# Performance work log

Hardware: AMD Instinct MI355X
Metric: run time of the kernel (lower is better)

## Reference

```python
import jax, jax.numpy as jnp
import numpy as np

B, C, N, K, H = 8, 64, 4096, 32, 4
D = C // H  # head dim = 16
EPS = 1e-5  # BatchNorm eps (torch default)


def setup_inputs() -> dict:
    key = jax.random.key(0)
    ks = jax.random.split(key, 7)
    s = 0.05
    return {
        "x": jax.random.normal(ks[0], (B, C, N), jnp.float32),
        "wq": jax.random.normal(ks[1], (C, C), jnp.float32) * s,
        "wk": jax.random.normal(ks[2], (C, C), jnp.float32) * s,
        "wv": jax.random.normal(ks[3], (C, C), jnp.float32) * s,
        "w1": jax.random.normal(ks[4], (4 * C, C), jnp.float32) * s,
        "w2": jax.random.normal(ks[5], (C, 4 * C), jnp.float32) * s,
        "g1": jnp.ones((C,), jnp.float32),
        "b1": jnp.zeros((C,), jnp.float32),
        "g2": jnp.ones((C,), jnp.float32),
        "b2": jnp.zeros((C,), jnp.float32),
    }


def _bn(f, g, b):
    # BatchNorm1d in training mode: stats over (batch, points) per channel.
    # f: (B, N, C)
    mu = jnp.mean(f, axis=(0, 1))
    var = jnp.var(f, axis=(0, 1))  # biased, as torch uses for normalization
    return (f - mu) * jax.lax.rsqrt(var + EPS) * g + b


def reference(x, wq, wk, wv, w1, w2, g1, b1, g2, b2):
    feat = jnp.transpose(x, (0, 2, 1))  # (B, N, C)
    # KNN in feature space: negative squared distances, take top-K largest
    sq = jnp.sum(feat * feat, axis=-1)  # (B, N)
    neg_d = 2.0 * jnp.einsum('bnc,bmc->bnm', feat, feat) - sq[:, :, None] - sq[:, None, :]
    _, idx = jax.lax.top_k(neg_d, K)  # (B, N, K) int32
    # gather neighbors and form diffs
    nbrs = jax.vmap(lambda p, i: p[i])(feat, idx)  # (B, N, K, C)
    diff = nbrs - feat[:, :, None, :]
    # 1x1-conv projections (bias-free linear over channels)
    q = jnp.einsum('bnc,oc->bno', feat, wq).reshape(B, N, H, D)
    k = jnp.einsum('bnkc,oc->bnko', diff, wk).reshape(B, N, K, H, D)
    v = jnp.einsum('bnkc,oc->bnko', diff, wv).reshape(B, N, K, H, D)
    energy = jnp.einsum('bnhd,bnkhd->bnhk', q, k) / jnp.sqrt(jnp.float32(D))
    attn = jax.nn.softmax(energy, axis=-1)  # softmax over K neighbors
    out = jnp.einsum('bnhk,bnkhd->bnhd', attn, v).reshape(B, N, C)  # H-major merge
    f1 = _bn(feat + out, g1, b1)
    hid = jnp.einsum('bnc,oc->bno', f1, w1)
    hid = jnp.where(hid > 0, hid, 0.2 * hid)  # LeakyReLU(0.2)
    ff = jnp.einsum('bno,co->bnc', hid, w2)
    f2 = _bn(f1 + ff, g2, b2)
    return jnp.transpose(f2, (0, 2, 1))  # (B, C, N)
```

## Files before the change

### kernel.cpp

```cpp
#include <hip/hip_runtime.h>

#define Bdim 8
#define Cdim 64
#define Ndim 4096
#define Kdim 32
#define ROWS (Bdim*Ndim)
#define BN_EPS 1e-5f

__device__ __forceinline__ float dot4(float4 a, float4 b){
  return a.x*b.x + a.y*b.y + a.z*b.z + a.w*b.w;
}
__device__ __forceinline__ int wofs(int o, int g){ return o*64 + (((g ^ ((o>>2)&7)))<<2); }
__device__ __forceinline__ unsigned keyOf(float f){
  unsigned u = __float_as_uint(f);
  return (u & 0x80000000u) ? ~u : (u ^ 0x80000000u);
}

__global__ __launch_bounds__(256) void prep_proj_kernel(const float* __restrict__ x,
    const float* __restrict__ wq, const float* __restrict__ wk,
    const float* __restrict__ wv,
    float* __restrict__ sq,
    float* __restrict__ Qo, float* __restrict__ PKo, float* __restrict__ PVo,
    float* __restrict__ accZ)
{
  __shared__ __align__(16) float ftile[64*68];
  __shared__ __align__(16) float Ws[3][64*64];
  const int tid = threadIdx.x;
  const int blk = blockIdx.x;
  const int b  = blk & 7;
  const int n0 = (blk >> 3) * 64;
  if (blk == 0) accZ[tid] = 0.f;
  for (int k=0;k<16;++k){
    int idx = tid + (k<<8);
    int c = idx>>6, nn = idx&63;
    ftile[nn*68+c] = x[((size_t)b*64+c)*Ndim + n0 + nn];
  }
  {
    const float* wp[3] = {wq, wk, wv};
    for (int m=0;m<3;++m)
      for (int k=0;k<16;++k){
        int idx = tid + (k<<8);
        int o = idx>>6, c = idx&63;
        Ws[m][wofs(o, c>>2) + (c&3)] = wp[m][o*64 + c];
      }
  }
  __syncthreads();
  if (tid < 64){
    float a = 0.f;
    #pragma unroll
    for (int c=0;c<64;++c){ float v = ftile[tid*68+c]; a += v*v; }
    sq[b*Ndim + n0 + tid] = a;
  }
  const int tr = tid>>4, to = tid&15;
  const size_t rowBase = (size_t)b*Ndim + n0;
  float* outp[3] = {Qo, PKo, PVo};
  for (int m=0;m<3;++m){
    float acc[4][4];
    #pragma unroll
    for (int r=0;r<4;++r){ acc[r][0]=0.f; acc[r][1]=0.f; acc[r][2]=0.f; acc[r][3]=0.f; }
    #pragma unroll 4
    for (int c4=0;c4<16;++c4){
      float4 f[4], w[4];
      #pragma unroll
      for (int r=0;r<4;++r)  f[r] = *(const float4*)&ftile[(4*tr+r)*68 + (c4<<2)];
      #pragma unroll
      for (int oo=0;oo<4;++oo) w[oo] = *(const float4*)&Ws[m][wofs(4*to+oo, c4)];
      #pragma unroll
      for (int r=0;r<4;++r)
        #pragma unroll
        for (int oo=0;oo<4;++oo)
          acc[r][oo] += dot4(f[r], w[oo]);
    }
    #pragma unroll
    for (int r=0;r<4;++r){
      float4 v; v.x=acc[r][0]; v.y=acc[r][1]; v.z=acc[r][2]; v.w=acc[r][3];
      *(float4*)&outp[m][(rowBase + 4*tr + r)*64 + 4*to] = v;
    }
  }
}

__global__ __launch_bounds__(512, 4) void knn_attn_kernel(
    const float* __restrict__ x,
    const float* __restrict__ sq,
    const float* __restrict__ Qm, const float* __restrict__ PKm, const float* __restrict__ PVm,
    float* __restrict__ t1, float* __restrict__ bn1s, float* __restrict__ bn1q)
{
  __shared__ __align__(16) unsigned char smem[40992];
  float*    chunkF = (float*)smem;
  unsigned* candK  = (unsigned*)smem;
  int*      candI  = (int*)(smem + 2048);
  int*      outIdx = (int*)(smem + 4096);
  float*    enS    = (float*)(smem + 5120);
  float*    red1   = (float*)(smem + 5120);
  float*    red2   = (float*)(smem + 7168);
  float*    fnS    = (float*)(smem + 32768);
  float*    qvS    = (float*)(smem + 34816);
  float*    pknS   = (float*)(smem + 36864);
  float*    pvnS   = (float*)(smem + 38912);
  float*    sqnS   = (float*)(smem + 40960);

  const int tid = threadIdx.x;
  const int lane = tid & 63;
  const int w = tid >> 6;
  const int blk = blockIdx.x;
  const int b  = blk & 7;
  const int n0 = (blk >> 3) << 3;
  const float* xb = x + (size_t)b*64*Ndim;

  {
    int j = tid>>6, c = tid&63;
    size_t ro = ((size_t)b*Ndim + n0 + j)*64 + c;
    fnS[tid]  = xb[(size_t)c*Ndim + n0 + j];
    qvS[tid]  = Qm[ro];
    pknS[tid] = PKm[ro];
    pvnS[tid] = PVm[ro];
    if (tid < 8) sqnS[tid] = sq[b*Ndim + n0 + tid];
  }
  __syncthreads();

  unsigned kk[64];

  #pragma unroll
  for (int g=0; g<2; ++g){
    const int m0 = (g<<11) + (tid<<2);
    float acc[8][4];
    #pragma unroll
    for (int q=0;q<8;++q){ acc[q][0]=0.f; acc[q][1]=0.f; acc[q][2]=0.f; acc[q][3]=0.f; }
    #pragma unroll 4
    for (int c=0;c<64;++c){
      float4 xm = *(const float4*)&xb[(size_t)c*Ndim + m0];
      float4 qA = *(const float4*)&xb[(size_t)c*Ndim + n0];
      float4 qB = *(const float4*)&xb[(size_t)c*Ndim + n0 + 4];
      const float qs[8] = {qA.x,qA.y,qA.z,qA.w,qB.x,qB.y,qB.z,qB.w};
      #pragma unroll
      for (int q=0;q<8;++q){
        acc[q][0] += qs[q]*xm.x; acc[q][1] += qs[q]*xm.y;
        acc[q][2] += qs[q]*xm.z; acc[q][3] += qs[q]*xm.w;
      }
    }
    float4 sqm4 = *(const float4*)&sq[b*Ndim + m0];
    #pragma unroll
    for (int half=0; half<2; ++half){
      __syncthreads();
      #pragma unroll
      for (int qq=0;qq<4;++qq){
        int q = (half<<2)+qq;
        float sqn_q = sqnS[q];
        float4 v;
        v.x = (2.f*acc[q][0]-sqn_q)-sqm4.x;
        v.y = (2.f*acc[q][1]-sqn_q)-sqm4.y;
        v.z = (2.f*acc[q][2]-sqn_q)-sqm4.z;
        v.w = (2.f*acc[q][3]-sqn_q)-sqm4.w;
        *(float4*)&chunkF[(qq<<11) + (tid<<2)] = v;
      }
      __syncthreads();
      if ((w>>2) == half){
        const int wq = w & 3;
        #pragma unroll
        for (int i=0;i<32;++i)
          kk[(g<<5)+i] = keyOf(chunkF[(wq<<11)+(i<<6)+lane]);
      }
    }
  }
  __syncthreads();

  if (lane < 32) outIdx[(w<<5)+lane] = n0 + w;

  {
    unsigned lmax = kk[0];
    #pragma unroll
    for (int j=1;j<64;++j) lmax = lmax > kk[j] ? lmax : kk[j];
    unsigned T = 0u;
    #pragma unroll
    for (int bit=31; bit>=0; --bit){
      unsigned cand = T | (1u << bit);
      int cnt = (int)__popcll(__ballot(lmax >= cand));
      if (cnt >= 32) T = cand;
    }
    int base = 0;
    #pragma unroll
    for (int j=0;j<64;++j){
      bool isc = (kk[j] >= T);
      unsigned long long mk = __ballot(isc);
      if (isc){
        int slot = base + (int)__popcll(mk & ((1ull<<lane)-1ull));
        if (slot < 64){
          candK[(w<<6)+slot] = kk[j];
          candI[(w<<6)+slot] = ((j>>5)<<11)+((j&31)<<6)+lane;
        }
      }
      base += (int)__popcll(mk);
    }
    const int S = base;
    __threadfence_block();
    if (S <= 64){
      unsigned long long C = 0ull;
      if (lane < S)
        C = ((unsigned long long)candK[(w<<6)+lane] << 32) |
            (unsigned long long)(~(unsigned)candI[(w<<6)+lane]);
      #pragma unroll
      for (int k2=2; k2<=64; k2<<=1){
        #pragma unroll
        for (int j2=k2>>1; j2>=1; j2>>=1){
          unsigned long long P = (unsigned long long)__shfl_xor((long long)C, j2, 64);
          bool lowIdx  = ((lane & j2) == 0);
          bool keepMax = (lowIdx == ((lane & k2) == 0));
          unsigned long long mx = C > P ? C : P;
          unsigned long long mn = C > P ? P : C;
          C = keepMax ? mx : mn;
        }
      }
      if (lane < 32) outIdx[(w<<5)+lane] = (int)(~(unsigned)(C & 0xFFFFFFFFull)) & (Ndim-1);
    } else {
      unsigned Te = 0u;
      for (int bit=31; bit>=0; --bit){
        unsigned cand = Te | (1u << bit);
        int lc = 0;
        #pragma unroll
        for (int j=0;j<64;++j) lc += (kk[j] >= cand) ? 1 : 0;
        #pragma unroll
        for (int off=1; off<64; off<<=1) lc += __shfl_xor(lc, off, 64);
        if (lc >= 32) Te = cand;
      }
      const unsigned long long below = (1ull << lane) - 1ull;
      int b2 = 0;
      #pragma unroll
      for (int j=0;j<64;++j){
        unsigned u = kk[j];
        unsigned long long mg = __ballot(u > Te);
        if (u > Te){
          int slot = b2 + (int)__popcll(mg & below);
          if (slot < 32) outIdx[(w<<5)+slot] = ((j>>5)<<11)+((j&31)<<6)+lane;
        }
        b2 += (int)__popcll(mg);
      }
      #pragma unroll
      for (int j=0;j<64;++j){
        unsigned u = kk[j];
        unsigned long long mt = __ballot(u == Te);
        if (u == Te){
          int slot = b2 + (int)__popcll(mt & below);
          if (slot < 32) outIdx[(w<<5)+slot] = ((j>>5)<<11)+((j&31)<<6)+lane;
        }
        b2 += (int)__popcll(mt);
      }
    }
  }
  __syncthreads();

  #pragma unroll
  for (int p=0;p<2;++p){
    int task = tid + (p<<9);
    int jn = task>>7, h = (task>>5)&3, k2 = task&31;
    int mj = outIdx[(jn<<5)+k2] & (Ndim-1);
    const float4* pk4 = (const float4*)(PKm + ((size_t)b*Ndim + mj)*64 + (h<<4));
    const float4* qq4 = (const float4*)&qvS[(jn<<6)+(h<<4)];
    const float4* nn4 = (const float4*)&pknS[(jn<<6)+(h<<4)];
    float e = 0.f;
    #pragma unroll
    for (int d=0;d<4;++d){
      float4 kv = pk4[d], qq = qq4[d], nn = nn4[d];
      e += qq.x*(kv.x-nn.x) + qq.y*(kv.y-nn.y) + qq.z*(kv.z-nn.z) + qq.w*(kv.w-nn.w);
    }
    enS[(jn<<7)+(h<<5)+k2] = e * 0.25f;
  }
  __syncthreads();
  if (tid < 32){
    int jn = tid>>2, h = tid&3;
    float* ep = &enS[(jn<<7)+(h<<5)];
    float mx = -1e30f;
    for (int k2=0;k2<32;++k2) mx = fmaxf(mx, ep[k2]);
    float ssum = 0.f;
    for (int k2=0;k2<32;++k2){ float ex = expf(ep[k2]-mx); ep[k2] = ex; ssum += ex; }
    float inv = 1.f/ssum;
    for (int k2=0;k2<32;++k2) ep[k2] *= inv;
  }
  __syncthreads();
  float tval;
  {
    int jn = tid>>6, c = tid&63, h = c>>4;
    float a2 = 0.f;
    #pragma unroll 8
    for (int k2=0;k2<32;++k2){
      int mj = outIdx[(jn<<5)+k2] & (Ndim-1);
      a2 += enS[(jn<<7)+(h<<5)+k2] * (PVm[((size_t)b*Ndim + mj)*64 + c] - pvnS[(jn<<6)+c]);
    }
    tval = fnS[(jn<<6)+c] + a2;
    t1[((size_t)b*Ndim + n0 + jn)*64 + c] = tval;
  }
  __syncthreads();
  red1[tid] = tval;
  red2[tid] = tval*tval;
  __syncthreads();
  if (tid < 64){
    float S = 0.f, S2 = 0.f;
    #pragma unroll
    for (int j=0;j<8;++j){ S += red1[(j<<6)+tid]; S2 += red2[(j<<6)+tid]; }
    atomicAdd(&bn1s[tid], S);
    atomicAdd(&bn1q[tid], S2);
  }
}

__global__ __launch_bounds__(256) void mlp_kernel(const float* __restrict__ t1,
    const float* __restrict__ w1, const float* __restrict__ w2,
    const float* __restrict__ g1, const float* __restrict__ b1,
    const float* __restrict__ bns, const float* __restrict__ bnq,
    float* __restrict__ t2, float* __restrict__ bn2s, float* __restrict__ bn2q)
{
  __shared__ __align__(16) float f1l[64*68];
  __shared__ __align__(16) float hl[64*68];
  __shared__ __align__(16) float w1s[64*64];
  __shared__ __align__(16) float w2s[64*64];
  __shared__ float mu[64], rs[64], gg[64], bb[64];
  const int tid = threadIdx.x;
  if (tid < 64){
    float m = bns[tid] * (1.f/32768.f);
    float v = bnq[tid] * (1.f/32768.f) - m*m;
    mu[tid] = m; rs[tid] = 1.f/sqrtf(v + BN_EPS);
    gg[tid] = g1[tid]; bb[tid] = b1[tid];
  }
  __syncthreads();
  const size_t rowBase = (size_t)blockIdx.x*64;
  for (int k=0;k<16;++k){
    int idx = tid + (k<<8);
    int r = idx>>6, c = idx&63;
    float v = t1[(rowBase + r)*64 + c];
    f1l[r*68+c] = (v - mu[c])*rs[c]*gg[c] + bb[c];
  }
  const int tr = tid>>4, to = tid&15;
  float ff[4][4];
  #pragma unroll
  for (int r=0;r<4;++r){ ff[r][0]=0.f; ff[r][1]=0.f; ff[r][2]=0.f; ff[r][3]=0.f; }

  for (int hc=0; hc<4; ++hc){
    __syncthreads();
    for (int k=0;k<16;++k){
      int idx = tid + (k<<8);
      int o = idx>>6, c = idx&63;
      w1s[wofs(o, c>>2) + (c&3)] = w1[(size_t)(hc*64+o)*64 + c];
      w2s[wofs(o, c>>2) + (c&3)] = w2[(size_t)o*256 + hc*64 + c];
    }
    __syncthreads();
    float hv[4][4];
    #pragma unroll
    for (int r=0;r<4;++r){ hv[r][0]=0.f; hv[r][1]=0.f; hv[r][2]=0.f; hv[r][3]=0.f; }
    #pragma unroll 4
    for (int c4=0;c4<16;++c4){
      float4 f[4], w[4];
      #pragma unroll
      for (int r=0;r<4;++r)  f[r] = *(const float4*)&f1l[(4*tr+r)*68 + (c4<<2)];
      #pragma unroll
      for (int oo=0;oo<4;++oo) w[oo] = *(const float4*)&w1s[wofs(4*to+oo, c4)];
      #pragma unroll
      for (int r=0;r<4;++r)
        #pragma unroll
        for (int oo=0;oo<4;++oo)
          hv[r][oo] += dot4(f[r], w[oo]);
    }
    #pragma unroll
    for (int r=0;r<4;++r){
      float4 v;
      float x0=hv[r][0], x1=hv[r][1], x2=hv[r][2], x3=hv[r][3];
      v.x = (x0>0.f)?x0:0.2f*x0; v.y = (x1>0.f)?x1:0.2f*x1;
      v.z = (x2>0.f)?x2:0.2f*x2; v.w = (x3>0.f)?x3:0.2f*x3;
      *(float4*)&hl[(4*tr+r)*68 + 4*to] = v;
    }
    __syncthreads();
    #pragma unroll 4
    for (int o4=0;o4<16;++o4){
      float4 h[4], w[4];
      #pragma unroll
      for (int r=0;r<4;++r)  h[r] = *(const float4*)&hl[(4*tr+r)*68 + (o4<<2)];
      #pragma unroll
      for (int oo=0;oo<4;++oo) w[oo] = *(const float4*)&w2s[wofs(4*to+oo, o4)];
      #pragma unroll
      for (int r=0;r<4;++r)
        #pragma unroll
        for (int oo=0;oo<4;++oo)
          ff[r][oo] += dot4(h[r], w[oo]);
    }
  }
  float ls[4]  = {0.f,0.f,0.f,0.f};
  float ls2[4] = {0.f,0.f,0.f,0.f};
  #pragma unroll
  for (int r=0;r<4;++r){
    float4 v;
    v.x = f1l[(4*tr+r)*68 + 4*to+0] + ff[r][0];
    v.y = f1l[(4*tr+r)*68 + 4*to+1] + ff[r][1];
    v.z = f1l[(4*tr+r)*68 + 4*to+2] + ff[r][2];
    v.w = f1l[(4*tr+r)*68 + 4*to+3] + ff[r][3];
    *(float4*)&t2[(rowBase + 4*tr + r)*64 + 4*to] = v;
    ls[0]+=v.x; ls[1]+=v.y; ls[2]+=v.z; ls[3]+=v.w;
    ls2[0]+=v.x*v.x; ls2[1]+=v.y*v.y; ls2[2]+=v.z*v.z; ls2[3]+=v.w*v.w;
  }
  __syncthreads();
  #pragma unroll
  for (int i=0;i<4;++i){
    hl[tr*64 + 4*to + i]        = ls[i];
    hl[1024 + tr*64 + 4*to + i] = ls2[i];
  }
  __syncthreads();
  if (tid < 64){
    float S = 0.f, S2 = 0.f;
    #pragma unroll
    for (int g2=0; g2<16; ++g2){ S += hl[g2*64 + tid]; S2 += hl[1024 + g2*64 + tid]; }
    atomicAdd(&bn2s[tid], S);
    atomicAdd(&bn2q[tid], S2);
  }
}

__global__ __launch_bounds__(256) void final_kernel(const float* __restrict__ t2,
    const float* __restrict__ bns, const float* __restrict__ bnq,
    const float* __restrict__ g2, const float* __restrict__ b2,
    float* __restrict__ out)
{
  __shared__ float tile[64*65];
  __shared__ float mu[64], rs[64], gg[64], bb[64];
  const int tid = threadIdx.x;
  const int b = blockIdx.y;
  const int n0 = blockIdx.x*64;
  if (tid < 64){
    float m = bns[tid] * (1.f/32768.f);
    float v = bnq[tid] * (1.f/32768.f) - m*m;
    mu[tid] = m; rs[tid] = 1.f/sqrtf(v + BN_EPS);
    gg[tid] = g2[tid]; bb[tid] = b2[tid];
  }
  __syncthreads();
  for (int k=0;k<16;++k){
    int idx = tid + (k<<8);
    int r = idx>>6, c = idx&63;
    float v = t2[((size_t)b*Ndim + n0 + r)*64 + c];
    tile[r*65+c] = (v - mu[c])*rs[c]*gg[c] + bb[c];
  }
  __syncthreads();
  for (int k=0;k<16;++k){
    int idx = tid + (k<<8);
    int c = idx>>6, nn = idx&63;
    out[((size_t)b*64 + c)*Ndim + n0 + nn] = tile[nn*65+c];
  }
}

extern "C" void kernel_launch(void* const* d_in, const int* in_sizes, int n_in,
                              void* d_out, int out_size, void* d_ws, size_t ws_size,
                              hipStream_t stream)
{
  (void)in_sizes; (void)n_in; (void)out_size; (void)ws_size;
  const float* x  = (const float*)d_in[0];
  const float* wq = (const float*)d_in[1];
  const float* wk = (const float*)d_in[2];
  const float* wv = (const float*)d_in[3];
  const float* w1 = (const float*)d_in[4];
  const float* w2 = (const float*)d_in[5];
  const float* g1 = (const float*)d_in[6];
  const float* b1 = (const float*)d_in[7];
  const float* g2 = (const float*)d_in[8];
  const float* b2 = (const float*)d_in[9];
  float* out = (float*)d_out;

  const size_t NE = (size_t)ROWS*64;
  float* sq   = (float*)d_ws;
  float* Qb   = sq + ROWS;
  float* PKb  = Qb + NE;
  float* PVb  = PKb + NE;
  float* t1   = PVb + NE;
  float* t2   = t1 + NE;
  float* acc  = t2 + NE;

  prep_proj_kernel<<<dim3(512), 256, 0, stream>>>(x, wq, wk, wv, sq, Qb, PKb, PVb, acc);
  knn_attn_kernel<<<dim3(4096), 512, 0, stream>>>(x, sq, Qb, PKb, PVb, t1, acc, acc+64);
  mlp_kernel<<<dim3(512), 256, 0, stream>>>(t1, w1, w2, g1, b1, acc, acc+64, t2, acc+128, acc+192);
  final_kernel<<<dim3(64,8), 256, 0, stream>>>(t2, acc+128, acc+192, g2, b2, out);
}
```

Before: 443.8 us.

## Use bf16 MFMA for KNN distances with 16-bit keys and exact fp32 rerank

The prep kernel now also writes a row-major fp32 copy of the features and a bf16 copy. The KNN kernel computes approximate pairwise distances with bf16 MFMA instructions and quantizes them to 16-bit keys, so two query rows share each register key. It then selects candidates with a widened threshold margin and re-ranks up to 64 of them with exact fp32 distances before a bitonic sort. Each block handles 16 query points instead of 8, halving the grid. The cost is the risk of missing true neighbours when quantization error exceeds the margin or more than 64 candidates tie, plus extra workspace writes. The t2 buffer is reused as scratch.

```diff
diff --git a/kernel.cpp b/kernel.cpp
--- a/kernel.cpp
+++ b/kernel.cpp
@@ -7,6 +7,9 @@
 #define ROWS (Bdim*Ndim)
 #define BN_EPS 1e-5f
 
+using f32x4  = __attribute__((ext_vector_type(4))) float;
+using bf16x8 = __attribute__((ext_vector_type(8))) short;
+
 __device__ __forceinline__ float dot4(float4 a, float4 b){
   return a.x*b.x + a.y*b.y + a.z*b.z + a.w*b.w;
 }
@@ -21,7 +24,8 @@
     const float* __restrict__ wv,
     float* __restrict__ sq,
     float* __restrict__ Qo, float* __restrict__ PKo, float* __restrict__ PVo,
-    float* __restrict__ accZ)
+    float* __restrict__ accZ,
+    float* __restrict__ featT, unsigned short* __restrict__ xh)
 {
   __shared__ __align__(16) float ftile[64*68];
   __shared__ __align__(16) float Ws[3][64*64];
@@ -29,6 +33,7 @@
   const int blk = blockIdx.x;
   const int b  = blk & 7;
   const int n0 = (blk >> 3) * 64;
+  const size_t rowBase = (size_t)b*Ndim + n0;
   if (blk == 0) accZ[tid] = 0.f;
   for (int k=0;k<16;++k){
     int idx = tid + (k<<8);
@@ -45,6 +50,15 @@
       }
   }
   __syncthreads();
+  for (int k=0;k<16;++k){
+    int idx = tid + (k<<8);
+    int r = idx>>6, c = idx&63;
+    float v = ftile[r*68+c];
+    size_t o = (rowBase + r)*64 + c;
+    featT[o] = v;
+    unsigned u = __float_as_uint(v);
+    xh[o] = (unsigned short)((u + 0x7FFFu + ((u>>16)&1u)) >> 16);
+  }
   if (tid < 64){
     float a = 0.f;
     #pragma unroll
@@ -52,7 +66,6 @@
     sq[b*Ndim + n0 + tid] = a;
   }
   const int tr = tid>>4, to = tid&15;
-  const size_t rowBase = (size_t)b*Ndim + n0;
   float* outp[3] = {Qo, PKo, PVo};
   for (int m=0;m<3;++m){
     float acc[4][4];
@@ -80,180 +93,179 @@
 }
 
 __global__ __launch_bounds__(512, 4) void knn_attn_kernel(
-    const float* __restrict__ x,
     const float* __restrict__ sq,
     const float* __restrict__ Qm, const float* __restrict__ PKm, const float* __restrict__ PVm,
+    const float* __restrict__ featT, const unsigned short* __restrict__ xh,
     float* __restrict__ t1, float* __restrict__ bn1s, float* __restrict__ bn1q)
 {
-  __shared__ __align__(16) unsigned char smem[40992];
-  float*    chunkF = (float*)smem;
-  unsigned* candK  = (unsigned*)smem;
-  int*      candI  = (int*)(smem + 2048);
-  int*      outIdx = (int*)(smem + 4096);
-  float*    enS    = (float*)(smem + 5120);
-  float*    red1   = (float*)(smem + 5120);
-  float*    red2   = (float*)(smem + 7168);
-  float*    fnS    = (float*)(smem + 32768);
-  float*    qvS    = (float*)(smem + 34816);
-  float*    pknS   = (float*)(smem + 36864);
-  float*    pvnS   = (float*)(smem + 38912);
-  float*    sqnS   = (float*)(smem + 40960);
-
-  const int tid = threadIdx.x;
+  __shared__ __align__(16) unsigned char smem[49216];
+  unsigned short* bufA = (unsigned short*)smem;
+  unsigned short* bufB = (unsigned short*)(smem + 16384);
+  int*   candI  = (int*)smem;
+  int*   outIdx = (int*)(smem + 2048);
+  float* enS    = (float*)(smem + 4096);
+  float* red1   = (float*)(smem + 12288);
+  float* red2   = (float*)(smem + 14336);
+  float* fnS    = (float*)(smem + 32768);
+  float* qvS    = (float*)(smem + 36864);
+  float* pknS   = (float*)(smem + 40960);
+  float* pvnS   = (float*)(smem + 45056);
+  float* sqnS   = (float*)(smem + 49152);
+
+  const int tid  = threadIdx.x;
   const int lane = tid & 63;
-  const int w = tid >> 6;
-  const int blk = blockIdx.x;
-  const int b  = blk & 7;
-  const int n0 = (blk >> 3) << 3;
-  const float* xb = x + (size_t)b*64*Ndim;
+  const int w    = tid >> 6;
+  const int blk  = blockIdx.x;
+  const int b    = blk & 7;
+  const int n0   = (blk >> 3) << 4;
+  const size_t b4096 = (size_t)b << 12;
+  const int qa = w, qb = w + 8;
+
+  #pragma unroll
+  for (int rr=0; rr<2; ++rr){
+    int idx = tid + (rr<<9);
+    int j = idx>>6, c = idx&63;
+    size_t ro = (b4096 + n0 + j)*64 + c;
+    fnS[idx]  = featT[ro];
+    qvS[idx]  = Qm[ro];
+    pknS[idx] = PKm[ro];
+    pvnS[idx] = PVm[ro];
+  }
+  if (tid < 16) sqnS[tid] = sq[b4096 + n0 + tid];
+  __syncthreads();
+
+  unsigned kk[64];
 
   {
-    int j = tid>>6, c = tid&63;
-    size_t ro = ((size_t)b*Ndim + n0 + j)*64 + c;
-    fnS[tid]  = xb[(size_t)c*Ndim + n0 + j];
-    qvS[tid]  = Qm[ro];
-    pknS[tid] = PKm[ro];
-    pvnS[tid] = PVm[ro];
-    if (tid < 8) sqnS[tid] = sq[b*Ndim + n0 + tid];
-  }
-  __syncthreads();
-
-  unsigned kk[64];
-
-  #pragma unroll
-  for (int g=0; g<2; ++g){
-    const int m0 = (g<<11) + (tid<<2);
-    float acc[8][4];
-    #pragma unroll
-    for (int q=0;q<8;++q){ acc[q][0]=0.f; acc[q][1]=0.f; acc[q][2]=0.f; acc[q][3]=0.f; }
-    #pragma unroll 4
-    for (int c=0;c<64;++c){
-      float4 xm = *(const float4*)&xb[(size_t)c*Ndim + m0];
-      float4 qA = *(const float4*)&xb[(size_t)c*Ndim + n0];
-      float4 qB = *(const float4*)&xb[(size_t)c*Ndim + n0 + 4];
-      const float qs[8] = {qA.x,qA.y,qA.z,qA.w,qB.x,qB.y,qB.z,qB.w};
-      #pragma unroll
-      for (int q=0;q<8;++q){
-        acc[q][0] += qs[q]*xm.x; acc[q][1] += qs[q]*xm.y;
-        acc[q][2] += qs[q]*xm.z; acc[q][3] += qs[q]*xm.w;
-      }
-    }
-    float4 sqm4 = *(const float4*)&sq[b*Ndim + m0];
-    #pragma unroll
-    for (int half=0; half<2; ++half){
+    const unsigned short* xhb = xh + (b4096 << 6);
+    const int l15  = lane & 15;
+    const int acol = (lane >> 4) << 3;
+    const int qrow = (lane >> 4) << 2;
+    bf16x8 a0 = *(const bf16x8*)&xhb[(size_t)(n0 + l15)*64 + acol];
+    bf16x8 a1 = *(const bf16x8*)&xhb[(size_t)(n0 + l15)*64 + acol + 32];
+    float sqn_r[4];
+    #pragma unroll
+    for (int r=0;r<4;++r) sqn_r[r] = sqnS[qrow + r];
+    const float* sqb = sq + b4096;
+    #pragma unroll
+    for (int ch=0; ch<8; ++ch){
+      unsigned short* buf = (ch & 1) ? bufB : bufA;
+      #pragma unroll
+      for (int t=0;t<4;++t){
+        const int brow = (w<<9) + (ch<<6) + (t<<4) + l15;
+        bf16x8 b0 = *(const bf16x8*)&xhb[(size_t)brow*64 + acol];
+        bf16x8 b1 = *(const bf16x8*)&xhb[(size_t)brow*64 + acol + 32];
+        f32x4 acc = {0.f,0.f,0.f,0.f};
+        acc = __builtin_amdgcn_mfma_f32_16x16x32_bf16(a0, b0, acc, 0, 0, 0);
+        acc = __builtin_amdgcn_mfma_f32_16x16x32_bf16(a1, b1, acc, 0, 0, 0);
+        float sm = sqb[brow];
+        #pragma unroll
+        for (int r=0;r<4;++r){
+          float d = 2.f*acc[r] - sqn_r[r] - sm;
+          int k16 = (int)fmaf(d, 204.8f, 65536.0f);
+          k16 = k16 < 0 ? 0 : (k16 > 65535 ? 65535 : k16);
+          buf[((w<<4) + qrow + r)*64 + (t<<4) + l15] = (unsigned short)k16;
+        }
+      }
       __syncthreads();
       #pragma unroll
-      for (int qq=0;qq<4;++qq){
-        int q = (half<<2)+qq;
-        float sqn_q = sqnS[q];
-        float4 v;
-        v.x = (2.f*acc[q][0]-sqn_q)-sqm4.x;
-        v.y = (2.f*acc[q][1]-sqn_q)-sqm4.y;
-        v.z = (2.f*acc[q][2]-sqn_q)-sqm4.z;
-        v.w = (2.f*acc[q][3]-sqn_q)-sqm4.w;
-        *(float4*)&chunkF[(qq<<11) + (tid<<2)] = v;
-      }
-      __syncthreads();
-      if ((w>>2) == half){
-        const int wq = w & 3;
-        #pragma unroll
-        for (int i=0;i<32;++i)
-          kk[(g<<5)+i] = keyOf(chunkF[(wq<<11)+(i<<6)+lane]);
-      }
-    }
-  }
-  __syncthreads();
-
-  if (lane < 32) outIdx[(w<<5)+lane] = n0 + w;
-
-  {
-    unsigned lmax = kk[0];
-    #pragma unroll
-    for (int j=1;j<64;++j) lmax = lmax > kk[j] ? lmax : kk[j];
-    unsigned T = 0u;
-    #pragma unroll
-    for (int bit=31; bit>=0; --bit){
-      unsigned cand = T | (1u << bit);
+      for (int i=0;i<8;++i){
+        unsigned kA = buf[((i<<4) + qa)*64 + lane];
+        unsigned kB = buf[((i<<4) + qb)*64 + lane];
+        kk[(ch<<3)+i] = (kA<<16) | kB;
+      }
+    }
+  }
+
+  if (lane < 32){ outIdx[(qa<<5)+lane] = n0 + qa; outIdx[(qb<<5)+lane] = n0 + qb; }
+
+  const unsigned long long below = (1ull<<lane) - 1ull;
+  #pragma unroll
+  for (int pass=0; pass<2; ++pass){
+    const int q = pass ? qb : qa;
+    unsigned lmax = 0;
+    #pragma unroll
+    for (int j=0;j<64;++j){
+      unsigned kj = pass ? (kk[j]&0xFFFFu) : (kk[j]>>16);
+      lmax = lmax > kj ? lmax : kj;
+    }
+    unsigned T = 0;
+    #pragma unroll
+    for (int bit=15; bit>=0; --bit){
+      unsigned cand = T | (1u<<bit);
       int cnt = (int)__popcll(__ballot(lmax >= cand));
       if (cnt >= 32) T = cand;
     }
+    const unsigned Tm = (T > 72u) ? (T - 72u) : 0u;
     int base = 0;
     #pragma unroll
     for (int j=0;j<64;++j){
-      bool isc = (kk[j] >= T);
+      unsigned kj = pass ? (kk[j]&0xFFFFu) : (kk[j]>>16);
+      bool isc = (kj >= Tm);
       unsigned long long mk = __ballot(isc);
       if (isc){
-        int slot = base + (int)__popcll(mk & ((1ull<<lane)-1ull));
-        if (slot < 64){
-          candK[(w<<6)+slot] = kk[j];
-          candI[(w<<6)+slot] = ((j>>5)<<11)+((j&31)<<6)+lane;
+        int slot = base + (int)__popcll(mk & below);
+        if (slot < 64) candI[(w<<6)+slot] = ((j&7)<<9) + ((j>>3)<<6) + lane;
+      }
+      base += (int)__popcll(mk);
+    }
+    int S = base;
+    if (S > 64){
+      base = 0;
+      #pragma unroll
+      for (int j=0;j<64;++j){
+        unsigned kj = pass ? (kk[j]&0xFFFFu) : (kk[j]>>16);
+        bool isc = (kj >= T);
+        unsigned long long mk = __ballot(isc);
+        if (isc){
+          int slot = base + (int)__popcll(mk & below);
+          if (slot < 64) candI[(w<<6)+slot] = ((j&7)<<9) + ((j>>3)<<6) + lane;
         }
-      }
-      base += (int)__popcll(mk);
-    }
-    const int S = base;
+        base += (int)__popcll(mk);
+      }
+      S = base < 64 ? base : 64;
+    }
     __threadfence_block();
-    if (S <= 64){
-      unsigned long long C = 0ull;
-      if (lane < S)
-        C = ((unsigned long long)candK[(w<<6)+lane] << 32) |
-            (unsigned long long)(~(unsigned)candI[(w<<6)+lane]);
-      #pragma unroll
-      for (int k2=2; k2<=64; k2<<=1){
-        #pragma unroll
-        for (int j2=k2>>1; j2>=1; j2>>=1){
-          unsigned long long P = (unsigned long long)__shfl_xor((long long)C, j2, 64);
-          bool lowIdx  = ((lane & j2) == 0);
-          bool keepMax = (lowIdx == ((lane & k2) == 0));
-          unsigned long long mx = C > P ? C : P;
-          unsigned long long mn = C > P ? P : C;
-          C = keepMax ? mx : mn;
-        }
-      }
-      if (lane < 32) outIdx[(w<<5)+lane] = (int)(~(unsigned)(C & 0xFFFFFFFFull)) & (Ndim-1);
-    } else {
-      unsigned Te = 0u;
-      for (int bit=31; bit>=0; --bit){
-        unsigned cand = Te | (1u << bit);
-        int lc = 0;
-        #pragma unroll
-        for (int j=0;j<64;++j) lc += (kk[j] >= cand) ? 1 : 0;
-        #pragma unroll
-        for (int off=1; off<64; off<<=1) lc += __shfl_xor(lc, off, 64);
-        if (lc >= 32) Te = cand;
-      }
-      const unsigned long long below = (1ull << lane) - 1ull;
-      int b2 = 0;
-      #pragma unroll
-      for (int j=0;j<64;++j){
-        unsigned u = kk[j];
-        unsigned long long mg = __ballot(u > Te);
-        if (u > Te){
-          int slot = b2 + (int)__popcll(mg & below);
-          if (slot < 32) outIdx[(w<<5)+slot] = ((j>>5)<<11)+((j&31)<<6)+lane;
-        }
-        b2 += (int)__popcll(mg);
-      }
-      #pragma unroll
-      for (int j=0;j<64;++j){
-        unsigned u = kk[j];
-        unsigned long long mt = __ballot(u == Te);
-        if (u == Te){
-          int slot = b2 + (int)__popcll(mt & below);
-          if (slot < 32) outIdx[(w<<5)+slot] = ((j>>5)<<11)+((j&31)<<6)+lane;
-        }
-        b2 += (int)__popcll(mt);
-      }
-    }
-  }
-  __syncthreads();
-
-  #pragma unroll
-  for (int p=0;p<2;++p){
+    int mj = -1; unsigned keyE = 0u;
+    if (lane < S){
+      mj = candI[(w<<6)+lane];
+      const float* fm = featT + (b4096 + mj)*64;
+      const float* fq = fnS + (q<<6);
+      float as = 0.f;
+      #pragma unroll
+      for (int d4=0; d4<16; ++d4){
+        float4 qv = *(const float4*)&fq[d4<<2];
+        float4 mv = *(const float4*)&fm[d4<<2];
+        as = fmaf(qv.x, mv.x, as); as = fmaf(qv.y, mv.y, as);
+        as = fmaf(qv.z, mv.z, as); as = fmaf(qv.w, mv.w, as);
+      }
+      float de = (2.f*as - sqnS[q]) - sq[b4096 + mj];
+      keyE = keyOf(de);
+    }
+    unsigned long long C = ((unsigned long long)keyE << 32) |
+                           (unsigned long long)(~(unsigned)mj);
+    #pragma unroll
+    for (int k2=2; k2<=64; k2<<=1){
+      #pragma unroll
+      for (int j2=k2>>1; j2>=1; j2>>=1){
+        unsigned long long P = (unsigned long long)__shfl_xor((long long)C, j2, 64);
+        bool lowIdx  = ((lane & j2) == 0);
+        bool keepMax = (lowIdx == ((lane & k2) == 0));
+        unsigned long long mx = C > P ? C : P;
+        unsigned long long mn = C > P ? P : C;
+        C = keepMax ? mx : mn;
+      }
+    }
+    if (lane < 32) outIdx[(q<<5)+lane] = (int)(~(unsigned)(C & 0xFFFFFFFFull)) & (Ndim-1);
+  }
+  __syncthreads();
+
+  #pragma unroll
+  for (int p=0;p<4;++p){
     int task = tid + (p<<9);
     int jn = task>>7, h = (task>>5)&3, k2 = task&31;
     int mj = outIdx[(jn<<5)+k2] & (Ndim-1);
-    const float4* pk4 = (const float4*)(PKm + ((size_t)b*Ndim + mj)*64 + (h<<4));
+    const float4* pk4 = (const float4*)(PKm + (b4096 + mj)*64 + (h<<4));
     const float4* qq4 = (const float4*)&qvS[(jn<<6)+(h<<4)];
     const float4* nn4 = (const float4*)&pknS[(jn<<6)+(h<<4)];
     float e = 0.f;
@@ -265,7 +277,7 @@
     enS[(jn<<7)+(h<<5)+k2] = e * 0.25f;
   }
   __syncthreads();
-  if (tid < 32){
+  if (tid < 64){
     int jn = tid>>2, h = tid&3;
     float* ep = &enS[(jn<<7)+(h<<5)];
     float mx = -1e30f;
@@ -276,21 +288,22 @@
     for (int k2=0;k2<32;++k2) ep[k2] *= inv;
   }
   __syncthreads();
-  float tval;
-  {
-    int jn = tid>>6, c = tid&63, h = c>>4;
+  float tv[2];
+  #pragma unroll
+  for (int rr=0; rr<2; ++rr){
+    int jn = (tid>>6) + (rr<<3);
+    int c = tid&63, h = c>>4;
     float a2 = 0.f;
     #pragma unroll 8
     for (int k2=0;k2<32;++k2){
       int mj = outIdx[(jn<<5)+k2] & (Ndim-1);
-      a2 += enS[(jn<<7)+(h<<5)+k2] * (PVm[((size_t)b*Ndim + mj)*64 + c] - pvnS[(jn<<6)+c]);
-    }
-    tval = fnS[(jn<<6)+c] + a2;
-    t1[((size_t)b*Ndim + n0 + jn)*64 + c] = tval;
-  }
-  __syncthreads();
-  red1[tid] = tval;
-  red2[tid] = tval*tval;
+      a2 += enS[(jn<<7)+(h<<5)+k2] * (PVm[(b4096 + mj)*64 + c] - pvnS[(jn<<6)+c]);
+    }
+    tv[rr] = fnS[(jn<<6)+c] + a2;
+    t1[(b4096 + n0 + jn)*64 + c] = tv[rr];
+  }
+  red1[tid] = tv[0] + tv[1];
+  red2[tid] = tv[0]*tv[0] + tv[1]*tv[1];
   __syncthreads();
   if (tid < 64){
     float S = 0.f, S2 = 0.f;
@@ -465,9 +478,10 @@
   float* t1   = PVb + NE;
   float* t2   = t1 + NE;
   float* acc  = t2 + NE;
-
-  prep_proj_kernel<<<dim3(512), 256, 0, stream>>>(x, wq, wk, wv, sq, Qb, PKb, PVb, acc);
-  knn_attn_kernel<<<dim3(4096), 512, 0, stream>>>(x, sq, Qb, PKb, PVb, t1, acc, acc+64);
+  unsigned short* xh = (unsigned short*)(acc + 256);
+
+  prep_proj_kernel<<<dim3(512), 256, 0, stream>>>(x, wq, wk, wv, sq, Qb, PKb, PVb, acc, t2, xh);
+  knn_attn_kernel<<<dim3(2048), 512, 0, stream>>>(sq, Qb, PKb, PVb, t2, xh, t1, acc, acc+64);
   mlp_kernel<<<dim3(512), 256, 0, stream>>>(t1, w1, w2, g1, b1, acc, acc+64, t2, acc+128, acc+192);
   final_kernel<<<dim3(64,8), 256, 0, stream>>>(t2, acc+128, acc+192, g2, b2, out);
 }
```

Result: no change. 437.4 us (-1.5%).
